# Performance work log

Hardware: AMD Instinct MI355X
Metric: run time of the kernel (lower is better)

## Reference

```python
import jax, jax.numpy as jnp
import numpy as np

LAYER_NAMES = ["self", "cross", "self", "cross", "self", "cross"]
L = len(LAYER_NAMES)
D = 256          # feature_dim
H = 4            # num_heads
HEAD_DIM = D // H
BS = 2           # image pairs
N = 1024         # keypoints per image
BN_EPS = 1e-5


def _conv1x1(x, W, b):
    # x: [B, Cin, N], W: [Cout, Cin] -> [B, Cout, N]  (Conv1d kernel_size=1)
    return jnp.einsum('oi,bin->bon', W, x) + b[None, :, None]


def _batchnorm1d(x, gamma, beta):
    # training-mode BatchNorm1d over [B, C, N]: stats over (B, N) per channel
    mean = jnp.mean(x, axis=(0, 2), keepdims=True)
    var = jnp.var(x, axis=(0, 2), keepdims=True)
    return (x - mean) * jax.lax.rsqrt(var + BN_EPS) * gamma[None, :, None] + beta[None, :, None]


def _attention(q_in, k_in, v_in, mask, Wq, bq, Wk, bk, Wv, bv, Wm, bm):
    B = q_in.shape[0]
    q = _conv1x1(q_in, Wq, bq).reshape(B, HEAD_DIM, H, -1)   # [B, d, h, n]
    k = _conv1x1(k_in, Wk, bk).reshape(B, HEAD_DIM, H, -1)
    v = _conv1x1(v_in, Wv, bv).reshape(B, HEAD_DIM, H, -1)
    scores = jnp.einsum('bdhn,bdhm->bhnm', q, k) / (HEAD_DIM ** 0.5)
    # multiplicative mask (NOT additive), applied before softmax
    scores = scores * mask[:, None, :, :]
    prob = jax.nn.softmax(scores, axis=-1)
    x = jnp.einsum('bhnm,bdhm->bdhn', prob, v)               # [B, d, h, n]
    return _conv1x1(x.reshape(B, D, -1), Wm, bm)             # merge


def _gnn(desc0, desc1, M0, M1, Wq, bq, Wk, bk, Wv, bv, Wm, bm, W1, b1, g1, beta1, W2, b2):
    bs = desc0.shape[0]
    mask = jnp.concatenate([M0, M1], axis=0)                 # [2bs, N, N]
    for i, name in enumerate(LAYER_NAMES):
        x = jnp.concatenate([desc0, desc1], axis=0)          # [2bs, D, N]
        src = jnp.concatenate([desc1, desc0], axis=0) if name == 'cross' else x
        message = _attention(x, src, src, mask,
                             Wq[i], bq[i], Wk[i], bk[i], Wv[i], bv[i], Wm[i], bm[i])
        y = jnp.concatenate([x, message], axis=1)            # [2bs, 2D, N]
        y = jax.nn.relu(_batchnorm1d(_conv1x1(y, W1[i], b1[i]), g1[i], beta1[i]))
        delta = _conv1x1(y, W2[i], b2[i])                    # [2bs, D, N]
        desc0 = desc0 + delta[:bs]
        desc1 = desc1 + delta[bs:]
    # concat the two updated descriptor sets along batch for a single output array
    return jnp.concatenate([desc0, desc1], axis=0)


def setup_inputs() -> dict:
    key = jax.random.key(0)
    ks = jax.random.split(key, 12)
    s = 0.02
    return {
        'desc0': jax.random.normal(ks[0], (BS, D, N), jnp.float32),
        'desc1': jax.random.normal(ks[1], (BS, D, N), jnp.float32),
        'M0': jnp.ones((BS, N, N), jnp.float32),
        'M1': jnp.ones((BS, N, N), jnp.float32),
        'Wq': jax.random.normal(ks[2], (L, D, D), jnp.float32) * s,
        'bq': jnp.zeros((L, D), jnp.float32),
        'Wk': jax.random.normal(ks[3], (L, D, D), jnp.float32) * s,
        'bk': jnp.zeros((L, D), jnp.float32),
        'Wv': jax.random.normal(ks[4], (L, D, D), jnp.float32) * s,
        'bv': jnp.zeros((L, D), jnp.float32),
        'Wm': jax.random.normal(ks[5], (L, D, D), jnp.float32) * s,
        'bm': jnp.zeros((L, D), jnp.float32),
        'W1': jax.random.normal(ks[6], (L, 2 * D, 2 * D), jnp.float32) * s,
        'b1': jnp.zeros((L, 2 * D), jnp.float32),
        'g1': jnp.ones((L, 2 * D), jnp.float32),
        'beta1': jnp.zeros((L, 2 * D), jnp.float32),
        'W2': jax.random.normal(ks[7], (L, D, 2 * D), jnp.float32) * s,
        'b2': jnp.zeros((L, D), jnp.float32),
    }


def reference(desc0, desc1, M0, M1, Wq, bq, Wk, bk, Wv, bv, Wm, bm, W1, b1, g1, beta1, W2, b2):
    return _gnn(desc0, desc1, M0, M1, Wq, bq, Wk, bk, Wv, bv, Wm, bm, W1, b1, g1, beta1, W2, b2)
```

## Files before the change

### kernel.cpp

```cpp
#include <hip/hip_runtime.h>
#include <hip/hip_bf16.h>

#define NN 1024
#define DD 256
#define LL 6

typedef __attribute__((ext_vector_type(8))) short bf16x8;
typedef __attribute__((ext_vector_type(4))) float f32x4;
typedef __attribute__((ext_vector_type(4))) unsigned short u16x4;

__device__ __forceinline__ unsigned short f2bf(float f) {
    union { float f; unsigned u; } x; x.f = f;
    return (unsigned short)((x.u + 0x7fffu + ((x.u >> 16) & 1u)) >> 16);
}

__device__ __forceinline__ float bf2f(unsigned short u) {
    union { unsigned u; float f; } x; x.u = ((unsigned)u) << 16; return x.f;
}

__device__ __forceinline__ f32x4 mfma16(bf16x8 a, bf16x8 b, f32x4 c) {
    return __builtin_amdgcn_mfma_f32_16x16x32_bf16(a, b, c, 0, 0, 0);
}

__device__ __forceinline__ void gll16(const unsigned short* g, unsigned short* l) {
    __builtin_amdgcn_global_load_lds(
        (const __attribute__((address_space(1))) unsigned int*)g,
        (__attribute__((address_space(3))) unsigned int*)l, 16, 0, 0);
}

__global__ __launch_bounds__(256) void prep_kernel(
    const float* __restrict__ desc0, const float* __restrict__ desc1,
    const float* __restrict__ M0, const float* __restrict__ M1,
    const float* __restrict__ Wq, const float* __restrict__ Wk,
    const float* __restrict__ Wv, const float* __restrict__ Wm,
    const float* __restrict__ W1, const float* __restrict__ W2,
    const float* __restrict__ bm, const float* __restrict__ b1,
    unsigned short* __restrict__ wbf, unsigned short* __restrict__ maskbf,
    float* __restrict__ bmix, float* __restrict__ desc, unsigned short* __restrict__ xbf) {
    __shared__ float T[32][33];
    const int SQ = LL * 65536;
    const int S1 = LL * 262144;
    int blk = blockIdx.x, tid = threadIdx.x;
    if (blk < 15360) {
        int idx = blk * 256 + tid;
        int total = 4 * SQ + S1 + LL * 131072;
        if (idx >= total) return;
        float v;
        if (idx < 4 * SQ) {
            int seg = idx / SQ, off = idx % SQ;
            const float* p = (seg == 0) ? Wq : (seg == 1) ? Wk : (seg == 2) ? Wv : Wm;
            if (seg < 3) {
                int l = off >> 16, rem = off & 65535;
                int op = rem >> 8, i = rem & 255;
                int src = ((op & 63) << 2) | (op >> 6);
                v = p[(size_t)l * 65536 + src * 256 + i];
            } else v = p[off];
        } else if (idx < 4 * SQ + S1) v = W1[idx - 4 * SQ];
        else v = W2[idx - 4 * SQ - S1];
        wbf[idx] = f2bf(v);
    } else if (blk < 19456) {
        int idx = (blk - 15360) * 256 + tid;
        size_t base = (size_t)idx * 4;
        int bb = (int)(base >> 20);
        const float* src = (bb < 2) ? (M0 + base) : (M1 + base - (2ull << 20));
        f32x4 v = *(const f32x4*)src;
        u16x4 o;
#pragma unroll
        for (int j = 0; j < 4; j++) o[j] = f2bf(v[j]);
        *(u16x4*)(maskbf + base) = o;
    } else if (blk < 20224) {
        int lane = tid & 63;
        int wid = (blk - 19456) * 4 + (tid >> 6);
        int l = wid >> 9, o = wid & 511;
        const float* row = W1 + ((size_t)l * 512 + o) * 512 + 256;
        const float* bmr = bm + (size_t)l * 256;
        f32x4 r = *(const f32x4*)(row + lane * 4);
        f32x4 b4 = *(const f32x4*)(bmr + lane * 4);
        float acc = r[0] * b4[0] + r[1] * b4[1] + r[2] * b4[2] + r[3] * b4[3];
        acc += __shfl_xor(acc, 1, 64);
        acc += __shfl_xor(acc, 2, 64);
        acc += __shfl_xor(acc, 4, 64);
        acc += __shfl_xor(acc, 8, 64);
        acc += __shfl_xor(acc, 16, 64);
        acc += __shfl_xor(acc, 32, 64);
        if (lane == 0) bmix[wid] = b1[wid] + acc;
    } else {
        int task = blk - 20224;
        int bb = task >> 8, tt = task & 255;
        int n0 = (tt >> 3) * 32, c0 = (tt & 7) * 32;
        const float* src = (bb < 2) ? (desc0 + (size_t)bb * DD * NN)
                                    : (desc1 + (size_t)(bb - 2) * DD * NN);
        int i = tid >> 5, j = tid & 31;
#pragma unroll
        for (int r = 0; r < 4; r++) {
            int c = i + r * 8;
            T[c][j] = src[(size_t)(c0 + c) * NN + n0 + j];
        }
        __syncthreads();
#pragma unroll
        for (int r = 0; r < 4; r++) {
            int n = i + r * 8;
            float v = T[j][n];
            size_t di = ((size_t)bb * NN + n0 + n) * DD + c0 + j;
            desc[di] = v;
            xbf[di] = f2bf(v);
        }
    }
}

__global__ __launch_bounds__(256) void fold1_kernel(const unsigned short* __restrict__ W1bf,
                                                    const unsigned short* __restrict__ Wmbf,
                                                    unsigned short* __restrict__ W1m) {
    int l = blockIdx.z;
    int o0 = blockIdx.x * 64, i0 = blockIdx.y * 64;
    const unsigned short* A = W1bf + (size_t)l * 262144;
    const unsigned short* B = Wmbf + (size_t)l * 65536;
    __shared__ unsigned short Bt[64][264];
    int t = threadIdx.x;
#pragma unroll
    for (int r = 0; r < 8; r++) {
        int j = r * 32 + (t >> 3);
        int il = (t & 7) * 8;
        union { bf16x8 v; unsigned short u[8]; } ld;
        ld.v = *(const bf16x8*)(B + (size_t)j * 256 + i0 + il);
#pragma unroll
        for (int jj = 0; jj < 8; jj++) Bt[il + jj][j] = ld.u[jj];
    }
    __syncthreads();
    int w = t >> 6, lane = t & 63, quad = lane >> 4, l15 = lane & 15;
    int wr = (w & 1) * 32, wc = (w >> 1) * 32;
    const unsigned short* Ab = A + (size_t)(o0 + wr + l15) * 512 + 256 + quad * 8;
    f32x4 acc[2][2];
#pragma unroll
    for (int r = 0; r < 2; r++)
#pragma unroll
        for (int c = 0; c < 2; c++) acc[r][c] = (f32x4){0.f, 0.f, 0.f, 0.f};
#pragma unroll
    for (int s = 0; s < 8; s++) {
        int kk = s * 32;
        bf16x8 a0 = *(const bf16x8*)(Ab + kk);
        bf16x8 a1 = *(const bf16x8*)(Ab + 16 * 512 + kk);
        bf16x8 b0 = *(const bf16x8*)(&Bt[wc + l15][kk + quad * 8]);
        bf16x8 b1 = *(const bf16x8*)(&Bt[wc + 16 + l15][kk + quad * 8]);
        acc[0][0] = mfma16(a0, b0, acc[0][0]);
        acc[0][1] = mfma16(a0, b1, acc[0][1]);
        acc[1][0] = mfma16(a1, b0, acc[1][0]);
        acc[1][1] = mfma16(a1, b1, acc[1][1]);
    }
#pragma unroll
    for (int rs = 0; rs < 2; rs++)
#pragma unroll
        for (int cs = 0; cs < 2; cs++)
#pragma unroll
            for (int reg = 0; reg < 4; reg++) {
                int o = o0 + wr + rs * 16 + quad * 4 + reg;
                int i = i0 + wc + cs * 16 + l15;
                int pc = (i & 3) * 64 + (i >> 2);
                W1m[((size_t)l * 512 + o) * 256 + pc] = f2bf(acc[rs][cs][reg]);
            }
}

__global__ __launch_bounds__(256) void final_kernel(const float* __restrict__ desc,
                                                    float* __restrict__ out) {
    __shared__ float T[32][33];
    int bb = blockIdx.z;
    int n0 = blockIdx.x * 32, c0 = blockIdx.y * 32;
    int i = threadIdx.x >> 5, j = threadIdx.x & 31;
#pragma unroll
    for (int r = 0; r < 4; r++) {
        int n = i + r * 8;
        T[n][j] = desc[((size_t)bb * NN + n0 + n) * DD + c0 + j];
    }
    __syncthreads();
#pragma unroll
    for (int r = 0; r < 4; r++) {
        int c = i + r * 8;
        out[((size_t)bb * DD + c0 + c) * NN + n0 + j] = T[j][c];
    }
}

__global__ __launch_bounds__(256) void proj_kernel(
    const unsigned short* __restrict__ xbf,
    const unsigned short* __restrict__ Wq_l, const unsigned short* __restrict__ Wk_l,
    const unsigned short* __restrict__ Wv_l,
    const float* __restrict__ bq_l, const float* __restrict__ bk_l,
    const float* __restrict__ bv_l,
    unsigned short* __restrict__ qb, unsigned short* __restrict__ kb,
    unsigned short* __restrict__ vb, int cross) {
    __shared__ __align__(16) unsigned short sm[8192];
    unsigned short* Al = sm;
    unsigned short* Bl = sm + 4096;

    int m0 = blockIdx.x * 64;
    int by = blockIdx.y;
    int mat = by >> 2;
    int o0c = (by & 3) * 64;
    int bb = m0 >> 10, nloc0 = m0 & 1023;
    int srcbb = (mat == 0) ? bb : (cross ? (bb ^ 2) : bb);
    const unsigned short* A = xbf + (size_t)srcbb * NN * DD + (size_t)nloc0 * DD;
    const unsigned short* W = ((mat == 0) ? Wq_l : (mat == 1) ? Wk_l : Wv_l) + (size_t)o0c * DD;
    const float* bias = (mat == 0) ? bq_l : (mat == 1) ? bk_l : bv_l;

    int tid = threadIdx.x, w = tid >> 6, lane = tid & 63, quad = lane >> 4, l15 = lane & 15;
    int wrow = (w & 1) * 32, wcol = (w >> 1) * 32;
    int lrow = lane >> 3, lcol = (lane & 7) * 8;

    f32x4 acc[2][2];
#pragma unroll
    for (int r = 0; r < 2; r++)
#pragma unroll
        for (int c = 0; c < 2; c++) acc[r][c] = (f32x4){0.f, 0.f, 0.f, 0.f};

    for (int ks = 0; ks < 4; ks++) {
        int k0 = ks * 64;
        __syncthreads();
#pragma unroll
        for (int j = 0; j < 2; j++)
            gll16(A + (size_t)(w * 16 + j * 8 + lrow) * DD + k0 + lcol, Al + (w * 16 + j * 8) * 64);
#pragma unroll
        for (int j = 0; j < 2; j++)
            gll16(W + (size_t)(w * 16 + j * 8 + lrow) * DD + k0 + lcol, Bl + (w * 16 + j * 8) * 64);
        __syncthreads();
#pragma unroll
        for (int kh = 0; kh < 2; kh++) {
            bf16x8 bf[2], af[2];
#pragma unroll
            for (int cs = 0; cs < 2; cs++)
                bf[cs] = *(const bf16x8*)(Bl + (wcol + cs * 16 + l15) * 64 + kh * 32 + quad * 8);
#pragma unroll
            for (int rs = 0; rs < 2; rs++)
                af[rs] = *(const bf16x8*)(Al + (wrow + rs * 16 + l15) * 64 + kh * 32 + quad * 8);
#pragma unroll
            for (int rs = 0; rs < 2; rs++)
#pragma unroll
                for (int cs = 0; cs < 2; cs++)
                    acc[rs][cs] = mfma16(af[rs], bf[cs], acc[rs][cs]);
        }
    }
    __syncthreads();
    float qscale = (mat == 0) ? 0.125f : 1.0f;
    if (mat < 2) {
#pragma unroll
        for (int rs = 0; rs < 2; rs++)
#pragma unroll
            for (int cs = 0; cs < 2; cs++) {
                int op = o0c + wcol + cs * 16 + l15;
                float bv4 = bias[((op & 63) << 2) | (op >> 6)];
#pragma unroll
                for (int reg = 0; reg < 4; reg++)
                    sm[(wrow + rs * 16 + quad * 4 + reg) * 72 + wcol + cs * 16 + l15] =
                        f2bf((acc[rs][cs][reg] + bv4) * qscale);
            }
        __syncthreads();
        int r = tid >> 2, ch = (tid & 3) * 16;
        unsigned short* dst = ((mat == 0) ? qb : kb) + ((size_t)(bb * NN) + nloc0 + r) * 256 + o0c + ch;
        *(bf16x8*)(dst) = *(const bf16x8*)(&sm[r * 72 + ch]);
        *(bf16x8*)(dst + 8) = *(const bf16x8*)(&sm[r * 72 + ch + 8]);
    } else {
#pragma unroll
        for (int rs = 0; rs < 2; rs++)
#pragma unroll
            for (int cs = 0; cs < 2; cs++) {
                int op = o0c + wcol + cs * 16 + l15;
                float bv4 = bias[((op & 63) << 2) | (op >> 6)];
#pragma unroll
                for (int reg = 0; reg < 4; reg++)
                    sm[(wcol + cs * 16 + l15) * 72 + wrow + rs * 16 + quad * 4 + reg] =
                        f2bf(acc[rs][cs][reg] + bv4);
            }
        __syncthreads();
        int o = tid >> 2, nch = (tid & 3) * 16;
        int opg = o0c + o;
        unsigned short* dst = vb + ((size_t)(bb * 4 + (opg >> 6)) * 64 + (opg & 63)) * NN + nloc0 + nch;
        *(bf16x8*)(dst) = *(const bf16x8*)(&sm[o * 72 + nch]);
        *(bf16x8*)(dst + 8) = *(const bf16x8*)(&sm[o * 72 + nch + 8]);
    }
}

__global__ __launch_bounds__(512, 4) void flash_kernel(
    const unsigned short* __restrict__ qb, const unsigned short* __restrict__ kb,
    const unsigned short* __restrict__ vb,
    const unsigned short* __restrict__ maskbf,
    unsigned short* __restrict__ xattn, float* __restrict__ bnsumm) {
    __shared__ __align__(16) char smem[51200];
    unsigned short* Plds = (unsigned short*)smem;
    float* OL = (float*)smem;

    int bh = blockIdx.y, nb = blockIdx.x;
    int bb = bh >> 2, h = bh & 3;
    int tid = threadIdx.x, w = tid >> 6, lane = tid & 63, quad = lane >> 4, l15 = lane & 15;
    int qg = w & 1, sp = w >> 1;

    if (nb == 0 && bh == 0) { bnsumm[tid] = 0.f; bnsumm[tid + 512] = 0.f; }

    const unsigned short* mask = maskbf + (size_t)bb * NN * NN;
    const unsigned short* Q = qb + (size_t)bb * NN * 256 + h * 64;
    const unsigned short* Kb = kb + (size_t)bb * NN * 256 + h * 64;
    const unsigned short* Vb = vb + (size_t)bh * 64 * NN;
    int row0 = nb * 32 + qg * 16;

    bf16x8 qf[2];
#pragma unroll
    for (int kc = 0; kc < 2; kc++)
        qf[kc] = *(const bf16x8*)(Q + (size_t)(row0 + l15) * 256 + kc * 32 + quad * 8);

    const unsigned short* mrow[4];
#pragma unroll
    for (int reg = 0; reg < 4; reg++)
        mrow[reg] = mask + (size_t)(row0 + quad * 4 + reg) * NN + sp * 256;

    f32x4 Oa[4];
#pragma unroll
    for (int dt = 0; dt < 4; dt++) Oa[dt] = (f32x4){0.f, 0.f, 0.f, 0.f};
    float mrun[4], lrun[4];
#pragma unroll
    for (int r = 0; r < 4; r++) { mrun[r] = -1e30f; lrun[r] = 0.f; }

    unsigned short* Pw = Plds + w * (16 * 72);

    for (int mt = 0; mt < 4; mt++) {
        int ml = mt * 64;
        int m0 = sp * 256 + ml;
        f32x4 s4[4];
#pragma unroll
        for (int t = 0; t < 4; t++) s4[t] = (f32x4){0.f, 0.f, 0.f, 0.f};
#pragma unroll
        for (int t = 0; t < 4; t++)
#pragma unroll
            for (int kc = 0; kc < 2; kc++) {
                bf16x8 kf = *(const bf16x8*)(Kb + (size_t)(m0 + t * 16 + l15) * 256 + kc * 32 + quad * 8);
                s4[t] = mfma16(qf[kc], kf, s4[t]);
            }
        bf16x8 vf[8];
#pragma unroll
        for (int dt = 0; dt < 4; dt++)
#pragma unroll
            for (int kc = 0; kc < 2; kc++)
                vf[dt * 2 + kc] = *(const bf16x8*)(Vb + (size_t)(dt * 16 + l15) * NN + m0 + kc * 32 + quad * 8);
        float sv[4][4], rmax[4];
#pragma unroll
        for (int r = 0; r < 4; r++) rmax[r] = -1e30f;
#pragma unroll
        for (int t = 0; t < 4; t++)
#pragma unroll
            for (int reg = 0; reg < 4; reg++) {
                float v = s4[t][reg] * bf2f(mrow[reg][ml + t * 16 + l15]);
                sv[t][reg] = v;
                rmax[reg] = fmaxf(rmax[reg], v);
            }
#pragma unroll
        for (int reg = 0; reg < 4; reg++) {
            rmax[reg] = fmaxf(rmax[reg], __shfl_xor(rmax[reg], 1, 64));
            rmax[reg] = fmaxf(rmax[reg], __shfl_xor(rmax[reg], 2, 64));
            rmax[reg] = fmaxf(rmax[reg], __shfl_xor(rmax[reg], 4, 64));
            rmax[reg] = fmaxf(rmax[reg], __shfl_xor(rmax[reg], 8, 64));
        }
        float alpha[4], rsum[4];
#pragma unroll
        for (int reg = 0; reg < 4; reg++) {
            float mn = fmaxf(mrun[reg], rmax[reg]);
            alpha[reg] = __expf(mrun[reg] - mn);
            mrun[reg] = mn;
            rsum[reg] = 0.f;
        }
#pragma unroll
        for (int t = 0; t < 4; t++)
#pragma unroll
            for (int reg = 0; reg < 4; reg++) {
                float p = __expf(sv[t][reg] - mrun[reg]);
                sv[t][reg] = p;
                rsum[reg] += p;
            }
#pragma unroll
        for (int reg = 0; reg < 4; reg++) {
            rsum[reg] += __shfl_xor(rsum[reg], 1, 64);
            rsum[reg] += __shfl_xor(rsum[reg], 2, 64);
            rsum[reg] += __shfl_xor(rsum[reg], 4, 64);
            rsum[reg] += __shfl_xor(rsum[reg], 8, 64);
            lrun[reg] = lrun[reg] * alpha[reg] + rsum[reg];
        }
#pragma unroll
        for (int dt = 0; dt < 4; dt++)
#pragma unroll
            for (int reg = 0; reg < 4; reg++) Oa[dt][reg] *= alpha[reg];
#pragma unroll
        for (int t = 0; t < 4; t++)
#pragma unroll
            for (int reg = 0; reg < 4; reg++)
                Pw[(quad * 4 + reg) * 72 + t * 16 + l15] = f2bf(sv[t][reg]);
        bf16x8 pf[2];
#pragma unroll
        for (int kc = 0; kc < 2; kc++)
            pf[kc] = *(const bf16x8*)(Pw + l15 * 72 + kc * 32 + quad * 8);
#pragma unroll
        for (int dt = 0; dt < 4; dt++)
#pragma unroll
            for (int kc = 0; kc < 2; kc++)
                Oa[dt] = mfma16(pf[kc], vf[dt * 2 + kc], Oa[dt]);
    }
    __syncthreads();
    float* mine = OL + (size_t)(w * 64 + lane) * 25;
#pragma unroll
    for (int dt = 0; dt < 4; dt++)
#pragma unroll
        for (int reg = 0; reg < 4; reg++) mine[dt * 4 + reg] = Oa[dt][reg];
#pragma unroll
    for (int reg = 0; reg < 4; reg++) { mine[16 + reg] = mrun[reg]; mine[20 + reg] = lrun[reg]; }
    __syncthreads();
    if (sp == 0) {
        const float* p[4];
#pragma unroll
        for (int j = 0; j < 4; j++) p[j] = OL + (size_t)((qg + 2 * j) * 64 + lane) * 25;
        float e[4][4], li[4];
#pragma unroll
        for (int reg = 0; reg < 4; reg++) {
            float M = fmaxf(fmaxf(p[0][16 + reg], p[1][16 + reg]),
                            fmaxf(p[2][16 + reg], p[3][16 + reg]));
            float L = 0.f;
#pragma unroll
            for (int j = 0; j < 4; j++) {
                e[j][reg] = __expf(p[j][16 + reg] - M);
                L += p[j][20 + reg] * e[j][reg];
            }
            li[reg] = 1.f / L;
        }
#pragma unroll
        for (int dt = 0; dt < 4; dt++)
#pragma unroll
            for (int reg = 0; reg < 4; reg++) {
                float val = 0.f;
#pragma unroll
                for (int j = 0; j < 4; j++) val += p[j][dt * 4 + reg] * e[j][reg];
                val *= li[reg];
                int n = row0 + quad * 4 + reg;
                int col = h * 64 + dt * 16 + l15;
                xattn[((size_t)bb * NN + n) * DD + col] = f2bf(val);
            }
    }
}

__global__ __launch_bounds__(256) void conv1_kernel(
    const unsigned short* __restrict__ xbf, const unsigned short* __restrict__ xattn,
    const unsigned short* __restrict__ W1_l, const unsigned short* __restrict__ W1m_l,
    const float* __restrict__ bmix_l,
    unsigned short* __restrict__ out1, float* __restrict__ bnsumm) {
    __shared__ __align__(16) unsigned short sm[8192];
    unsigned short* Al = sm;
    unsigned short* Bl = sm + 4096;

    int m0 = blockIdx.x * 64, o0 = blockIdx.y * 64;
    int bb = m0 >> 10, nloc0 = m0 & 1023;
    const unsigned short* A1 = xbf + (size_t)bb * NN * DD + (size_t)nloc0 * DD;
    const unsigned short* A2 = xattn + (size_t)bb * NN * DD + (size_t)nloc0 * DD;

    int tid = threadIdx.x, w = tid >> 6, lane = tid & 63, quad = lane >> 4, l15 = lane & 15;
    int wrow = (w & 1) * 32, wcol = (w >> 1) * 32;
    int lrow = lane >> 3, lcol = (lane & 7) * 8;

    f32x4 acc[2][2];
#pragma unroll
    for (int r = 0; r < 2; r++)
#pragma unroll
        for (int c = 0; c < 2; c++) acc[r][c] = (f32x4){0.f, 0.f, 0.f, 0.f};

    for (int ks = 0; ks < 8; ks++) {
        const unsigned short* As = (ks < 4) ? A1 : A2;
        int kloc = (ks & 3) * 64;
        __syncthreads();
#pragma unroll
        for (int j = 0; j < 2; j++)
            gll16(As + (size_t)(w * 16 + j * 8 + lrow) * DD + kloc + lcol, Al + (w * 16 + j * 8) * 64);
#pragma unroll
        for (int j = 0; j < 2; j++) {
            int orow = o0 + w * 16 + j * 8 + lrow;
            const unsigned short* bg = (ks < 4)
                ? (W1_l + (size_t)orow * 512 + ks * 64 + lcol)
                : (W1m_l + (size_t)orow * 256 + (ks - 4) * 64 + lcol);
            gll16(bg, Bl + (w * 16 + j * 8) * 64);
        }
        __syncthreads();
#pragma unroll
        for (int kh = 0; kh < 2; kh++) {
            bf16x8 bf[2], af[2];
#pragma unroll
            for (int cs = 0; cs < 2; cs++)
                bf[cs] = *(const bf16x8*)(Bl + (wcol + cs * 16 + l15) * 64 + kh * 32 + quad * 8);
#pragma unroll
            for (int rs = 0; rs < 2; rs++)
                af[rs] = *(const bf16x8*)(Al + (wrow + rs * 16 + l15) * 64 + kh * 32 + quad * 8);
#pragma unroll
            for (int rs = 0; rs < 2; rs++)
#pragma unroll
                for (int cs = 0; cs < 2; cs++)
                    acc[rs][cs] = mfma16(af[rs], bf[cs], acc[rs][cs]);
        }
    }
    __syncthreads();
    float cs_s[2] = {0.f, 0.f}, cs_q[2] = {0.f, 0.f};
#pragma unroll
    for (int rs = 0; rs < 2; rs++)
#pragma unroll
        for (int cs = 0; cs < 2; cs++) {
            int o = o0 + wcol + cs * 16 + l15;
            float bvx = bmix_l[o];
#pragma unroll
            for (int reg = 0; reg < 4; reg++) {
                float val = acc[rs][cs][reg] + bvx;
                sm[(wrow + rs * 16 + quad * 4 + reg) * 72 + wcol + cs * 16 + l15] = f2bf(val);
                cs_s[cs] += val;
                cs_q[cs] += val * val;
            }
        }
#pragma unroll
    for (int cs = 0; cs < 2; cs++) {
        cs_s[cs] += __shfl_xor(cs_s[cs], 16, 64);
        cs_s[cs] += __shfl_xor(cs_s[cs], 32, 64);
        cs_q[cs] += __shfl_xor(cs_q[cs], 16, 64);
        cs_q[cs] += __shfl_xor(cs_q[cs], 32, 64);
    }
    if (lane < 16) {
#pragma unroll
        for (int cs = 0; cs < 2; cs++) {
            atomicAdd(&bnsumm[o0 + wcol + cs * 16 + lane], cs_s[cs]);
            atomicAdd(&bnsumm[512 + o0 + wcol + cs * 16 + lane], cs_q[cs]);
        }
    }
    __syncthreads();
    int r = tid >> 2, ch = (tid & 3) * 16;
    unsigned short* dst = out1 + ((size_t)(bb * NN) + nloc0 + r) * 512 + o0 + ch;
    *(bf16x8*)(dst) = *(const bf16x8*)(&sm[r * 72 + ch]);
    *(bf16x8*)(dst + 8) = *(const bf16x8*)(&sm[r * 72 + ch + 8]);
}

__global__ __launch_bounds__(256) void bnrelu_kernel(
    const unsigned short* __restrict__ out1, const float* __restrict__ bnsumm,
    const float* __restrict__ g1_l, const float* __restrict__ beta1_l,
    unsigned short* __restrict__ ybf) {
    int idx = blockIdx.x * 256 + threadIdx.x;
    int base = idx * 8;
    int o = base & 511;
    union { bf16x8 v; unsigned short u[8]; } in, op;
    in.v = *(const bf16x8*)(out1 + base);
#pragma unroll
    for (int j = 0; j < 8; j++) {
        int ch = o + j;
        float s = bnsumm[ch], s2 = bnsumm[512 + ch];
        float mean = s * (1.f / 4096.f);
        float var = s2 * (1.f / 4096.f) - mean * mean;
        float sc = g1_l[ch] * rsqrtf(var + 1e-5f);
        float sh = beta1_l[ch] - mean * sc;
        op.u[j] = f2bf(fmaxf(0.f, bf2f(in.u[j]) * sc + sh));
    }
    *(bf16x8*)(ybf + base) = op.v;
}

__global__ __launch_bounds__(256) void conv2_kernel(
    const unsigned short* __restrict__ ybf, const unsigned short* __restrict__ W2_l,
    const float* __restrict__ b2_l, float* __restrict__ desc,
    unsigned short* __restrict__ xbf) {
    __shared__ __align__(16) unsigned short sm[6144];
    unsigned short* Al = sm;
    unsigned short* Bl = sm + 2048;

    int m0 = blockIdx.x * 32, o0 = blockIdx.y * 64;
    int bb = m0 >> 10, nloc0 = m0 & 1023;
    const unsigned short* A = ybf + ((size_t)(bb * NN) + nloc0) * 512;

    int tid = threadIdx.x, w = tid >> 6, lane = tid & 63, quad = lane >> 4, l15 = lane & 15;
    int wr = (w & 1) * 16, wc = (w >> 1) * 32;
    int lrow = lane >> 3, lcol = (lane & 7) * 8;

    f32x4 acc[2];
    acc[0] = (f32x4){0.f, 0.f, 0.f, 0.f};
    acc[1] = (f32x4){0.f, 0.f, 0.f, 0.f};

    for (int ks = 0; ks < 8; ks++) {
        int k0 = ks * 64;
        __syncthreads();
        gll16(A + (size_t)(w * 8 + lrow) * 512 + k0 + lcol, Al + (w * 8) * 64);
#pragma unroll
        for (int j = 0; j < 2; j++)
            gll16(W2_l + (size_t)(o0 + w * 16 + j * 8 + lrow) * 512 + k0 + lcol,
                  Bl + (w * 16 + j * 8) * 64);
        __syncthreads();
#pragma unroll
        for (int kh = 0; kh < 2; kh++) {
            bf16x8 af = *(const bf16x8*)(Al + (wr + l15) * 64 + kh * 32 + quad * 8);
#pragma unroll
            for (int cs = 0; cs < 2; cs++) {
                bf16x8 bf = *(const bf16x8*)(Bl + (wc + cs * 16 + l15) * 64 + kh * 32 + quad * 8);
                acc[cs] = mfma16(af, bf, acc[cs]);
            }
        }
    }
#pragma unroll
    for (int cs = 0; cs < 2; cs++)
#pragma unroll
        for (int reg = 0; reg < 4; reg++) {
            int n = nloc0 + wr + quad * 4 + reg;
            int o = o0 + wc + cs * 16 + l15;
            size_t di = ((size_t)bb * NN + n) * DD + o;
            float nd = desc[di] + acc[cs][reg] + b2_l[o];
            desc[di] = nd;
            xbf[di] = f2bf(nd);
        }
}

extern "C" void kernel_launch(void* const* d_in, const int* in_sizes, int n_in,
                              void* d_out, int out_size, void* d_ws, size_t ws_size,
                              hipStream_t stream) {
    const float* desc0 = (const float*)d_in[0];
    const float* desc1 = (const float*)d_in[1];
    const float* M0p   = (const float*)d_in[2];
    const float* M1p   = (const float*)d_in[3];
    const float* Wq = (const float*)d_in[4];  const float* bq = (const float*)d_in[5];
    const float* Wk = (const float*)d_in[6];  const float* bk = (const float*)d_in[7];
    const float* Wv = (const float*)d_in[8];  const float* bv = (const float*)d_in[9];
    const float* Wm = (const float*)d_in[10]; const float* bm = (const float*)d_in[11];
    const float* W1 = (const float*)d_in[12]; const float* b1 = (const float*)d_in[13];
    const float* g1 = (const float*)d_in[14]; const float* beta1 = (const float*)d_in[15];
    const float* W2 = (const float*)d_in[16]; const float* b2 = (const float*)d_in[17];
    float* out = (float*)d_out;
    char* ws = (char*)d_ws;

    float*          desc   = (float*)(ws);
    unsigned short* xbf    = (unsigned short*)(ws + (4ull << 20));
    unsigned short* qb     = (unsigned short*)(ws + (6ull << 20));
    unsigned short* kbuf   = (unsigned short*)(ws + (8ull << 20));
    unsigned short* vbuf   = (unsigned short*)(ws + (10ull << 20));
    unsigned short* xattn  = (unsigned short*)(ws + (12ull << 20));
    unsigned short* out1   = (unsigned short*)(ws + (14ull << 20));
    float*          bnsumm = (float*)(ws + (18ull << 20));
    float*          bmix   = (float*)(ws + (18ull << 20) + 8192);
    unsigned short* maskbf = (unsigned short*)(ws + (19ull << 20));
    unsigned short* W1m    = (unsigned short*)(ws + (27ull << 20));
    unsigned short* wbf    = (unsigned short*)(ws + (29ull << 20));
    unsigned short* ybf    = (unsigned short*)(ws + (37ull << 20));

    const int SQ = LL * 65536;

    prep_kernel<<<21248, 256, 0, stream>>>(desc0, desc1, M0p, M1p, Wq, Wk, Wv, Wm,
                                           W1, W2, bm, b1, wbf, maskbf, bmix, desc, xbf);
    fold1_kernel<<<dim3(8, 4, 6), 256, 0, stream>>>(wbf + 4 * (size_t)SQ, wbf + 3 * (size_t)SQ, W1m);

    for (int l = 0; l < LL; l++) {
        int cross = l & 1;
        const unsigned short* Wq_l = wbf + (size_t)l * 65536;
        const unsigned short* Wk_l = wbf + SQ + (size_t)l * 65536;
        const unsigned short* Wv_l = wbf + 2 * (size_t)SQ + (size_t)l * 65536;
        const unsigned short* W1_l = wbf + 4 * (size_t)SQ + (size_t)l * 262144;
        const unsigned short* W2_l = wbf + 4 * (size_t)SQ + (size_t)LL * 262144 + (size_t)l * 131072;
        const unsigned short* W1m_l = W1m + (size_t)l * 131072;

        proj_kernel<<<dim3(64, 12), 256, 0, stream>>>(
            xbf, Wq_l, Wk_l, Wv_l, bq + l * 256, bk + l * 256, bv + l * 256,
            qb, kbuf, vbuf, cross);
        flash_kernel<<<dim3(32, 16), 512, 0, stream>>>(qb, kbuf, vbuf, maskbf, xattn, bnsumm);
        conv1_kernel<<<dim3(64, 8), 256, 0, stream>>>(
            xbf, xattn, W1_l, W1m_l, bmix + l * 512, out1, bnsumm);
        bnrelu_kernel<<<1024, 256, 0, stream>>>(out1, bnsumm, g1 + l * 512, beta1 + l * 512, ybf);
        conv2_kernel<<<dim3(128, 4), 256, 0, stream>>>(
            ybf, W2_l, b2 + l * 256, desc, xbf);
    }

    final_kernel<<<dim3(32, 8, 4), 256, 0, stream>>>(desc, out);
}
```

Baseline: 512.0 us.

## Fuse weight folding into prep kernel and use exp2 softmax with log2e-scaled queries

The separate fold1 kernel (W1 times Wm product) becomes extra blocks in prep_kernel. Those blocks read the fp32 weights directly and convert them to bf16 on the fly, which removes one launch and the dependency on the bf16 weight copies. The query scale now folds in log2(e), so the flash softmax can use exp2f in place of __expf. Probabilities are stored to bf16 by truncation rather than round-to-nearest, which cuts a few ALU ops but adds a small downward rounding bias.

Result: slower. 537.6 us (+5.0%).

```diff
diff --git a/kernel.cpp b/kernel.cpp
--- a/kernel.cpp
+++ b/kernel.cpp
@@ -12,6 +12,11 @@
 __device__ __forceinline__ unsigned short f2bf(float f) {
     union { float f; unsigned u; } x; x.f = f;
     return (unsigned short)((x.u + 0x7fffu + ((x.u >> 16) & 1u)) >> 16);
+}
+
+__device__ __forceinline__ unsigned short f2bf_trunc(float f) {
+    union { float f; unsigned u; } x; x.f = f;
+    return (unsigned short)(x.u >> 16);
 }
 
 __device__ __forceinline__ float bf2f(unsigned short u) {
@@ -36,8 +41,9 @@
     const float* __restrict__ W1, const float* __restrict__ W2,
     const float* __restrict__ bm, const float* __restrict__ b1,
     unsigned short* __restrict__ wbf, unsigned short* __restrict__ maskbf,
-    float* __restrict__ bmix, float* __restrict__ desc, unsigned short* __restrict__ xbf) {
-    __shared__ float T[32][33];
+    float* __restrict__ bmix, float* __restrict__ desc, unsigned short* __restrict__ xbf,
+    unsigned short* __restrict__ W1m) {
+    __shared__ __align__(16) char pmem[17408];
     const int SQ = LL * 65536;
     const int S1 = LL * 262144;
     int blk = blockIdx.x, tid = threadIdx.x;
@@ -84,7 +90,8 @@
         acc += __shfl_xor(acc, 16, 64);
         acc += __shfl_xor(acc, 32, 64);
         if (lane == 0) bmix[wid] = b1[wid] + acc;
-    } else {
+    } else if (blk < 21248) {
+        float* T = (float*)pmem;
         int task = blk - 20224;
         int bb = task >> 8, tt = task & 255;
         int n0 = (tt >> 3) * 32, c0 = (tt & 7) * 32;
@@ -94,70 +101,78 @@
 #pragma unroll
         for (int r = 0; r < 4; r++) {
             int c = i + r * 8;
-            T[c][j] = src[(size_t)(c0 + c) * NN + n0 + j];
+            T[c * 33 + j] = src[(size_t)(c0 + c) * NN + n0 + j];
         }
         __syncthreads();
 #pragma unroll
         for (int r = 0; r < 4; r++) {
             int n = i + r * 8;
-            float v = T[j][n];
+            float v = T[j * 33 + n];
             size_t di = ((size_t)bb * NN + n0 + n) * DD + c0 + j;
             desc[di] = v;
             xbf[di] = f2bf(v);
         }
-    }
-}
-
-__global__ __launch_bounds__(256) void fold1_kernel(const unsigned short* __restrict__ W1bf,
-                                                    const unsigned short* __restrict__ Wmbf,
-                                                    unsigned short* __restrict__ W1m) {
-    int l = blockIdx.z;
-    int o0 = blockIdx.x * 64, i0 = blockIdx.y * 64;
-    const unsigned short* A = W1bf + (size_t)l * 262144;
-    const unsigned short* B = Wmbf + (size_t)l * 65536;
-    __shared__ unsigned short Bt[64][264];
-    int t = threadIdx.x;
-#pragma unroll
-    for (int r = 0; r < 8; r++) {
-        int j = r * 32 + (t >> 3);
-        int il = (t & 7) * 8;
-        union { bf16x8 v; unsigned short u[8]; } ld;
-        ld.v = *(const bf16x8*)(B + (size_t)j * 256 + i0 + il);
-#pragma unroll
-        for (int jj = 0; jj < 8; jj++) Bt[il + jj][j] = ld.u[jj];
-    }
-    __syncthreads();
-    int w = t >> 6, lane = t & 63, quad = lane >> 4, l15 = lane & 15;
-    int wr = (w & 1) * 32, wc = (w >> 1) * 32;
-    const unsigned short* Ab = A + (size_t)(o0 + wr + l15) * 512 + 256 + quad * 8;
-    f32x4 acc[2][2];
-#pragma unroll
-    for (int r = 0; r < 2; r++)
-#pragma unroll
-        for (int c = 0; c < 2; c++) acc[r][c] = (f32x4){0.f, 0.f, 0.f, 0.f};
-#pragma unroll
-    for (int s = 0; s < 8; s++) {
-        int kk = s * 32;
-        bf16x8 a0 = *(const bf16x8*)(Ab + kk);
-        bf16x8 a1 = *(const bf16x8*)(Ab + 16 * 512 + kk);
-        bf16x8 b0 = *(const bf16x8*)(&Bt[wc + l15][kk + quad * 8]);
-        bf16x8 b1 = *(const bf16x8*)(&Bt[wc + 16 + l15][kk + quad * 8]);
-        acc[0][0] = mfma16(a0, b0, acc[0][0]);
-        acc[0][1] = mfma16(a0, b1, acc[0][1]);
-        acc[1][0] = mfma16(a1, b0, acc[1][0]);
-        acc[1][1] = mfma16(a1, b1, acc[1][1]);
-    }
-#pragma unroll
-    for (int rs = 0; rs < 2; rs++)
-#pragma unroll
-        for (int cs = 0; cs < 2; cs++)
-#pragma unroll
-            for (int reg = 0; reg < 4; reg++) {
-                int o = o0 + wr + rs * 16 + quad * 4 + reg;
-                int i = i0 + wc + cs * 16 + l15;
-                int pc = (i & 3) * 64 + (i >> 2);
-                W1m[((size_t)l * 512 + o) * 256 + pc] = f2bf(acc[rs][cs][reg]);
-            }
+    } else {
+        unsigned short* Bt = (unsigned short*)pmem;
+        int w = tid >> 6, lane = tid & 63, quad = lane >> 4, l15 = lane & 15;
+        int wr = (w & 1) * 32, wc = (w >> 1) * 32;
+        int task = blk - 21248;
+        int l = task / 32, tt = task % 32;
+        int o0 = (tt >> 2) * 64, i0 = (tt & 3) * 64;
+        const float* A = W1 + (size_t)l * 262144;
+        const float* B = Wm + (size_t)l * 65536;
+        f32x4 acc[2][2];
+#pragma unroll
+        for (int r = 0; r < 2; r++)
+#pragma unroll
+            for (int c = 0; c < 2; c++) acc[r][c] = (f32x4){0.f, 0.f, 0.f, 0.f};
+        for (int ch = 0; ch < 2; ch++) {
+            __syncthreads();
+            int jj = tid >> 1, ih = (tid & 1) * 32;
+            const float* bs = B + (size_t)(ch * 128 + jj) * 256 + i0 + ih;
+#pragma unroll
+            for (int r = 0; r < 8; r++) {
+                f32x4 b4 = *(const f32x4*)(bs + r * 4);
+#pragma unroll
+                for (int q2 = 0; q2 < 4; q2++)
+                    Bt[(ih + r * 4 + q2) * 136 + jj] = f2bf(b4[q2]);
+            }
+            __syncthreads();
+#pragma unroll
+            for (int s = 0; s < 4; s++) {
+                bf16x8 af[2], bf[2];
+#pragma unroll
+                for (int rs = 0; rs < 2; rs++) {
+                    const float* ap = A + (size_t)(o0 + wr + rs * 16 + l15) * 512 + 256
+                                      + ch * 128 + s * 32 + quad * 8;
+                    f32x4 a04 = *(const f32x4*)ap;
+                    f32x4 a14 = *(const f32x4*)(ap + 4);
+                    union { bf16x8 v; unsigned short u[8]; } pk;
+#pragma unroll
+                    for (int jx = 0; jx < 4; jx++) { pk.u[jx] = f2bf(a04[jx]); pk.u[4 + jx] = f2bf(a14[jx]); }
+                    af[rs] = pk.v;
+                }
+#pragma unroll
+                for (int cs = 0; cs < 2; cs++)
+                    bf[cs] = *(const bf16x8*)(&Bt[(wc + cs * 16 + l15) * 136 + s * 32 + quad * 8]);
+                acc[0][0] = mfma16(af[0], bf[0], acc[0][0]);
+                acc[0][1] = mfma16(af[0], bf[1], acc[0][1]);
+                acc[1][0] = mfma16(af[1], bf[0], acc[1][0]);
+                acc[1][1] = mfma16(af[1], bf[1], acc[1][1]);
+            }
+        }
+#pragma unroll
+        for (int rs = 0; rs < 2; rs++)
+#pragma unroll
+            for (int cs = 0; cs < 2; cs++)
+#pragma unroll
+                for (int reg = 0; reg < 4; reg++) {
+                    int o = o0 + wr + rs * 16 + quad * 4 + reg;
+                    int i = i0 + wc + cs * 16 + l15;
+                    int pc = (i & 3) * 64 + (i >> 2);
+                    W1m[((size_t)l * 512 + o) * 256 + pc] = f2bf(acc[rs][cs][reg]);
+                }
+    }
 }
 
 __global__ __launch_bounds__(256) void final_kernel(const float* __restrict__ desc,
@@ -238,7 +253,7 @@
         }
     }
     __syncthreads();
-    float qscale = (mat == 0) ? 0.125f : 1.0f;
+    float qscale = (mat == 0) ? 0.1803368801f : 1.0f;
     if (mat < 2) {
 #pragma unroll
         for (int rs = 0; rs < 2; rs++)
@@ -359,7 +374,7 @@
 #pragma unroll
         for (int reg = 0; reg < 4; reg++) {
             float mn = fmaxf(mrun[reg], rmax[reg]);
-            alpha[reg] = __expf(mrun[reg] - mn);
+            alpha[reg] = exp2f(mrun[reg] - mn);
             mrun[reg] = mn;
             rsum[reg] = 0.f;
         }
@@ -367,7 +382,7 @@
         for (int t = 0; t < 4; t++)
 #pragma unroll
             for (int reg = 0; reg < 4; reg++) {
-                float p = __expf(sv[t][reg] - mrun[reg]);
+                float p = exp2f(sv[t][reg] - mrun[reg]);
                 sv[t][reg] = p;
                 rsum[reg] += p;
             }
@@ -387,7 +402,7 @@
         for (int t = 0; t < 4; t++)
 #pragma unroll
             for (int reg = 0; reg < 4; reg++)
-                Pw[(quad * 4 + reg) * 72 + t * 16 + l15] = f2bf(sv[t][reg]);
+                Pw[(quad * 4 + reg) * 72 + t * 16 + l15] = f2bf_trunc(sv[t][reg]);
         bf16x8 pf[2];
 #pragma unroll
         for (int kc = 0; kc < 2; kc++)
@@ -419,7 +434,7 @@
             float L = 0.f;
 #pragma unroll
             for (int j = 0; j < 4; j++) {
-                e[j][reg] = __expf(p[j][16 + reg] - M);
+                e[j][reg] = exp2f(p[j][16 + reg] - M);
                 L += p[j][20 + reg] * e[j][reg];
             }
             li[reg] = 1.f / L;
@@ -639,9 +654,8 @@
 
     const int SQ = LL * 65536;
 
-    prep_kernel<<<21248, 256, 0, stream>>>(desc0, desc1, M0p, M1p, Wq, Wk, Wv, Wm,
-                                           W1, W2, bm, b1, wbf, maskbf, bmix, desc, xbf);
-    fold1_kernel<<<dim3(8, 4, 6), 256, 0, stream>>>(wbf + 4 * (size_t)SQ, wbf + 3 * (size_t)SQ, W1m);
+    prep_kernel<<<21440, 256, 0, stream>>>(desc0, desc1, M0p, M1p, Wq, Wk, Wv, Wm,
+                                           W1, W2, bm, b1, wbf, maskbf, bmix, desc, xbf, W1m);
 
     for (int l = 0; l < LL; l++) {
         int cross = l & 1;
```
